# Performance work log

Measured on AMD Instinct MI355X. Metric: run time of the kernel, lower is better.

Reference implementation:

```python
import jax, jax.numpy as jnp
import numpy as np

S, B, D_MODEL, H = 2048, 2, 1024, 16
DH = D_MODEL // H
SCALE = 1.0 / np.sqrt(DH)
NEG_INF = jnp.float32(-1e30)


def setup_inputs() -> dict:
    key = jax.random.key(0)
    ks = jax.random.split(key, 12)
    std = 1.0 / np.sqrt(D_MODEL)
    inp = {
        "query": jax.random.normal(ks[0], (S, B, D_MODEL), jnp.float32),
        "key": jax.random.normal(ks[1], (S, B, D_MODEL), jnp.float32),
        "value": jax.random.normal(ks[2], (S, B, D_MODEL), jnp.float32),
        # causal mask, shape (seq_q, seq_k, 1) per prepare_mask asserts
        "mask": jnp.tril(jnp.ones((S, S), dtype=bool))[:, :, None],
        # params stored (in, out) for x @ W
        "Wq": jax.random.normal(ks[3], (D_MODEL, H * DH), jnp.float32) * std,
        "bq": jnp.zeros((H * DH,), jnp.float32),
        "Wk": jax.random.normal(ks[4], (D_MODEL, H * DH), jnp.float32) * std,
        "bk": jnp.zeros((H * DH,), jnp.float32),
        "Wv": jax.random.normal(ks[5], (D_MODEL, H * DH), jnp.float32) * std,
        "bv": jnp.zeros((H * DH,), jnp.float32),
        "Wo": jax.random.normal(ks[6], (D_MODEL, D_MODEL), jnp.float32) * std,
        "bo": jnp.zeros((D_MODEL,), jnp.float32),
    }
    return inp


def reference(query, key, value, mask, Wq, bq, Wk, bk, Wv, bv, Wo, bo):
    seq_len, batch, _ = query.shape
    # project and split heads: (S, B, H, DH)
    q = (query @ Wq + bq).reshape(seq_len, batch, H, DH)
    k = (key @ Wk + bk).reshape(key.shape[0], batch, H, DH)
    v = (value @ Wv + bv).reshape(value.shape[0], batch, H, DH)
    # scores: (seq_q, batch, heads, seq_k)
    scores = jnp.einsum("ibhd,jbhd->ibhj", q, k) * SCALE
    # mask (seq_q, seq_k, batch_or_1) -> broadcast to (seq_q, batch, 1, seq_k)
    m = jnp.transpose(mask, (0, 2, 1))[:, :, None, :]
    scores = jnp.where(m, scores, NEG_INF)
    attn = jax.nn.softmax(scores, axis=-1)  # dropout_prob=0.0 (eval)
    x = jnp.einsum("ibhj,jbhd->ibhd", attn, v)
    x = x.reshape(seq_len, batch, H * DH)
    return x @ Wo + bo
```

## Files before the change

### kernel.cpp

```cpp
#include <hip/hip_runtime.h>
#include <hip/hip_bf16.h>
#include <cstdint>

#define S_LEN 2048
#define BATCH 2
#define DM    1024
#define NH    16
#define DH    64

typedef short s8v __attribute__((ext_vector_type(8)));
typedef float f4v __attribute__((ext_vector_type(4)));
typedef unsigned int u32x2 __attribute__((ext_vector_type(2)));

__device__ __forceinline__ ushort f2bf(float x) {
  union { float f; uint32_t u; } v; v.f = x;
  uint32_t r = v.u + 0x7fffu + ((v.u >> 16) & 1u);
  return (ushort)(r >> 16);
}
__device__ __forceinline__ float bf2f(ushort u) {
  union { uint32_t u; float f; } v; v.u = (uint32_t)u << 16; return v.f;
}
__device__ __forceinline__ uint32_t fbits(float x) {
  union { float f; uint32_t u; } v; v.f = x; return v.u;
}
__device__ __forceinline__ uint32_t bfrnd(uint32_t u) {
  return u + 0x7fffu + ((u >> 16) & 1u);
}
__device__ __forceinline__ uint32_t packbf(uint32_t flo, uint32_t fhi) {
  return __builtin_amdgcn_perm(bfrnd(fhi), bfrnd(flo), 0x07060302u);
}
__device__ __forceinline__ uint32_t packbf_tr(float lo, float hi) {
  return __builtin_amdgcn_perm(fbits(hi), fbits(lo), 0x07060302u);
}

typedef __attribute__((address_space(1))) const void gas_void;
typedef __attribute__((address_space(3))) void las_void;
__device__ __forceinline__ void gld16(void* l, const void* g) {
  __builtin_amdgcn_global_load_lds((gas_void*)(uintptr_t)g,
                                   (las_void*)(uintptr_t)l, 16, 0, 0);
}

__global__ __launch_bounds__(256)
void prep(const float* W0, const float* W1, const float* W2, const float* W3,
          ushort* T0, ushort* T1, ushort* T2, ushort* T3,
          const float* X0, const float* X1, const float* X2,
          ushort* O0, ushort* O1, ushort* O2) {
  const int z = blockIdx.z;
  if (z < 4) {
    if (blockIdx.x >= 1024) return;
    const float* W = z == 0 ? W0 : z == 1 ? W1 : z == 2 ? W2 : W3;
    ushort*      T = z == 0 ? T0 : z == 1 ? T1 : z == 2 ? T2 : T3;
    __shared__ ushort tile[32][33];
    const int n0 = (blockIdx.x & 31) * 32, k0 = (blockIdx.x >> 5) * 32;
    const int tx = threadIdx.x & 31, ty = threadIdx.x >> 5;
    #pragma unroll
    for (int r = ty; r < 32; r += 8)
      tile[r][tx] = f2bf(W[(size_t)(k0 + r) * DM + n0 + tx]);
    __syncthreads();
    #pragma unroll
    for (int r = ty; r < 32; r += 8)
      T[(size_t)(n0 + r) * DM + k0 + tx] = tile[tx][r];
  } else {
    const float* X = z == 4 ? X0 : z == 5 ? X1 : X2;
    ushort*      O = z == 4 ? O0 : z == 5 ? O1 : O2;
    const size_t i = ((size_t)blockIdx.x * 256 + threadIdx.x) * 4;
    const float4 v = *(const float4*)(X + i);
    ushort4 h;
    h.x = f2bf(v.x); h.y = f2bf(v.y); h.z = f2bf(v.z); h.w = f2bf(v.w);
    *(ushort4*)(O + i) = h;
  }
}

__global__ __launch_bounds__(256, 2)
void gemm_qkv(const ushort* __restrict__ Xq, const ushort* __restrict__ Xk,
              const ushort* __restrict__ Xv,
              const ushort* __restrict__ Wqt, const ushort* __restrict__ Wkt,
              const ushort* __restrict__ Wvt,
              const float* __restrict__ bq, const float* __restrict__ bk,
              const float* __restrict__ bv,
              ushort* __restrict__ Qh, ushort* __restrict__ Kh,
              ushort* __restrict__ Vt) {
  const int z = blockIdx.z;
  const ushort* A    = z == 0 ? Xq  : z == 1 ? Xk  : Xv;
  const ushort* Bt   = z == 0 ? Wqt : z == 1 ? Wkt : Wvt;
  const float*  bias = z == 0 ? bq  : z == 1 ? bk  : bv;

  __shared__ __align__(16) ushort lds[32768];

  const int tid = threadIdx.x, lane = tid & 63, w = tid >> 6;
  const int wm = w >> 1, wn = w & 1;
  const int lrow = lane & 15, quad = lane >> 4;
  const int m0 = blockIdx.x * 128, n0 = blockIdx.y * 128;

  const int sr4 = lane >> 2;
  const int scol = ((lane & 3) ^ ((lane >> 3) & 3)) * 8;
  const ushort* gA[2]; const ushort* gB[2];
  int dA[2], dB[2];
  #pragma unroll
  for (int t = 0; t < 2; t++) {
    const int c = 2 * w + t;
    gA[t] = A  + (size_t)(m0 + c * 16 + sr4) * DM + scol;
    dA[t] = c * 512;
    gB[t] = Bt + (size_t)(n0 + c * 16 + sr4) * DM + scol;
    dB[t] = 4096 + c * 512;
  }

  const int fr = (lrow >> 1) & 3;
  int pa[4], pb[4];
  #pragma unroll
  for (int i = 0; i < 4; i++) {
    pa[i] = (wm * 64 + i * 16 + lrow) * 32 + ((quad ^ fr) * 8);
    pb[i] = 4096 + (wn * 64 + i * 16 + lrow) * 32 + ((quad ^ fr) * 8);
  }

  f4v acc[4][4];
  #pragma unroll
  for (int i = 0; i < 4; i++)
    #pragma unroll
    for (int j = 0; j < 4; j++)
      acc[i][j] = f4v{0.f, 0.f, 0.f, 0.f};

  #pragma unroll
  for (int t = 0; t < 3; t++) {
    const int bb = t * 8192, ko = t * 32;
    gld16(&lds[bb + dA[0]], gA[0] + ko);
    gld16(&lds[bb + dA[1]], gA[1] + ko);
    gld16(&lds[bb + dB[0]], gB[0] + ko);
    gld16(&lds[bb + dB[1]], gB[1] + ko);
  }
  asm volatile("s_waitcnt vmcnt(8)" ::: "memory");
  __builtin_amdgcn_s_barrier();

  for (int t = 0; t < 32; t++) {
    const int bb = (t & 3) * 8192;
    const bool st = t < 29;
    const int sbb = ((t + 3) & 3) * 8192;
    const int ko = (t + 3) * 32;
    s8v af[4], bf[4];
    #pragma unroll
    for (int i = 0; i < 4; i++) af[i] = *(const s8v*)&lds[bb + pa[i]];
    #pragma unroll
    for (int j = 0; j < 4; j++) bf[j] = *(const s8v*)&lds[bb + pb[j]];
    if (st) { gld16(&lds[sbb + dA[0]], gA[0] + ko); gld16(&lds[sbb + dA[1]], gA[1] + ko); }
    __builtin_amdgcn_s_barrier();
    __builtin_amdgcn_s_setprio(1);
    #pragma unroll
    for (int i = 0; i < 2; i++)
      #pragma unroll
      for (int j = 0; j < 4; j++)
        acc[i][j] = __builtin_amdgcn_mfma_f32_16x16x32_bf16(af[i], bf[j], acc[i][j], 0, 0, 0);
    __builtin_amdgcn_s_setprio(0);
    __builtin_amdgcn_s_barrier();
    if (st) { gld16(&lds[sbb + dB[0]], gB[0] + ko); gld16(&lds[sbb + dB[1]], gB[1] + ko); }
    __builtin_amdgcn_s_barrier();
    __builtin_amdgcn_s_setprio(1);
    #pragma unroll
    for (int i = 2; i < 4; i++)
      #pragma unroll
      for (int j = 0; j < 4; j++)
        acc[i][j] = __builtin_amdgcn_mfma_f32_16x16x32_bf16(af[i], bf[j], acc[i][j], 0, 0, 0);
    __builtin_amdgcn_s_setprio(0);
    if (t < 29)       asm volatile("s_waitcnt vmcnt(8)" ::: "memory");
    else if (t == 29) asm volatile("s_waitcnt vmcnt(4)" ::: "memory");
    else if (t == 30) asm volatile("s_waitcnt vmcnt(0)" ::: "memory");
    __builtin_amdgcn_s_barrier();
  }

  if (z <= 1) {
    ushort* O = (z == 0) ? Qh : Kh;
    #pragma unroll
    for (int i = 0; i < 4; i++)
      #pragma unroll
      for (int j = 0; j < 4; j++) {
        const int n = n0 + wn * 64 + j * 16 + lrow;
        const float bval = bias[n];
        const int h = n >> 6, d = n & 63;
        const int mb = m0 + wm * 64 + i * 16 + quad * 4;
        #pragma unroll
        for (int r = 0; r < 4; r++) {
          const int m = mb + r;
          O[((size_t)((m & 1) * NH + h) * S_LEN + (m >> 1)) * DH + d] = f2bf(acc[i][j][r] + bval);
        }
      }
  } else {
    ushort* tw = lds + w * 5120;
    const int h = (n0 + wn * 64) >> 6;
    const int s0 = (m0 + wm * 64) >> 1;
    #pragma unroll
    for (int i = 0; i < 4; i++)
      #pragma unroll
      for (int j = 0; j < 4; j++) {
        const int d_l = j * 16 + lrow;
        const float bval = bias[n0 + wn * 64 + d_l];
        const f4v a = acc[i][j];
        const int sbase = i * 8 + quad * 2;
        const uint32_t p0 = packbf(fbits(a[0] + bval), fbits(a[2] + bval));
        const uint32_t p1 = packbf(fbits(a[1] + bval), fbits(a[3] + bval));
        *(uint32_t*)&tw[d_l * 40 + sbase]        = p0;
        *(uint32_t*)&tw[2560 + d_l * 40 + sbase] = p1;
      }
    #pragma unroll
    for (int b = 0; b < 2; b++)
      #pragma unroll
      for (int p = 0; p < 4; p++) {
        const int d_l = p * 16 + (lane >> 2);
        const int c   = lane & 3;
        const s8v v = *(const s8v*)&tw[b * 2560 + d_l * 40 + c * 8];
        *(s8v*)&Vt[((size_t)(b * NH + h) * DH + d_l) * S_LEN + s0 + c * 8] = v;
      }
  }
}

__global__ __launch_bounds__(256)
void attn(const ushort* __restrict__ Qh, const ushort* __restrict__ Kh,
          const ushort* __restrict__ Vt, ushort* __restrict__ X,
          ushort* __restrict__ Opart, float* __restrict__ lpart) {
  __shared__ __align__(16) ushort lds[3 * 8192];

  const int tid = threadIdx.x, lane = tid & 63, w = tid >> 6;
  const int lrow = lane & 15, quad = lane >> 4;
  const int bh = blockIdx.x;
  const int slot = blockIdx.y;
  int qt, part, nparts;
  if (slot < 18)      { qt = 15 - slot / 3;        part = slot % 3;        nparts = 3; }
  else if (slot < 30) { qt = 9  - (slot - 18) / 2; part = (slot - 18) % 2; nparts = 2; }
  else                { qt = 33 - slot;            part = 0;               nparts = 1; }
  const int nj  = 2 * qt + 2;
  const int jlo = part * nj / nparts;
  const int jhi = (part + 1) * nj / nparts;
  const int iw  = qt * 128 + w * 32;

  const int srow = lane >> 3;
  const int scol = ((lane & 7) ^ srow) * 8;
  const ushort* gK0 = Kh + ((size_t)bh * S_LEN + 2 * w * 8 + srow) * DH + scol;
  const ushort* gK1 = gK0 + 8 * DH;
  const ushort* gV0 = Vt + ((size_t)bh * DH + 2 * w * 8 + srow) * S_LEN + scol;
  const ushort* gV1 = gV0 + 8 * S_LEN;
  const int lK0 = 2 * w * 512, lK1 = lK0 + 512;
  const int lV0 = 4096 + 2 * w * 512, lV1 = lV0 + 512;

  s8v aq[2][2];
  #pragma unroll
  for (int is = 0; is < 2; is++)
    #pragma unroll
    for (int kk = 0; kk < 2; kk++)
      aq[is][kk] = *(const s8v*)(Qh + ((size_t)bh * S_LEN + iw + is * 16 + lrow) * DH +
                                 kk * 32 + quad * 8);

  const int f8 = lrow & 7;
  int pk[4][2], pv[4][2];
  #pragma unroll
  for (int s4 = 0; s4 < 4; s4++)
    #pragma unroll
    for (int kk = 0; kk < 2; kk++) {
      pk[s4][kk] = (s4 * 16 + lrow) * 64 + (((kk * 4 + quad) ^ f8) * 8);
      pv[s4][kk] = 4096 + (s4 * 16 + lrow) * 64 + (((kk * 4 + quad) ^ f8) * 8);
    }

  f4v o[2][4];
  f4v lacc[2];
  #pragma unroll
  for (int is = 0; is < 2; is++) {
    lacc[is] = f4v{0.f, 0.f, 0.f, 0.f};
    #pragma unroll
    for (int d4 = 0; d4 < 4; d4++) o[is][d4] = f4v{0.f, 0.f, 0.f, 0.f};
  }
  const s8v vones = {0x3F80, 0x3F80, 0x3F80, 0x3F80, 0x3F80, 0x3F80, 0x3F80, 0x3F80};

  {
    const int b0 = (jlo % 3) * 8192;
    const size_t j0 = (size_t)jlo * 64;
    gld16(&lds[b0 + lK0], gK0 + j0 * DH);
    gld16(&lds[b0 + lK1], gK1 + j0 * DH);
    gld16(&lds[b0 + lV0], gV0 + j0);
    gld16(&lds[b0 + lV1], gV1 + j0);
    if (jlo + 1 < jhi) {
      const int b1 = ((jlo + 1) % 3) * 8192;
      const size_t j1 = (size_t)(jlo + 1) * 64;
      gld16(&lds[b1 + lK0], gK0 + j1 * DH);
      gld16(&lds[b1 + lK1], gK1 + j1 * DH);
      gld16(&lds[b1 + lV0], gV0 + j1);
      gld16(&lds[b1 + lV1], gV1 + j1);
    }
  }

  int bcur = jlo % 3;
  for (int jt = jlo; jt < jhi; jt++) {
    const int j0 = jt * 64;
    if (jt + 1 < jhi) asm volatile("s_waitcnt vmcnt(4)" ::: "memory");
    else              asm volatile("s_waitcnt vmcnt(0)" ::: "memory");
    __builtin_amdgcn_s_barrier();
    const int cur = bcur * 8192;
    if (jt + 2 < jhi) {
      const int sb = (bcur == 0 ? 2 : bcur - 1) * 8192;
      const size_t jn = (size_t)(jt + 2) * 64;
      gld16(&lds[sb + lK0], gK0 + jn * DH);
      gld16(&lds[sb + lK1], gK1 + jn * DH);
      gld16(&lds[sb + lV0], gV0 + jn);
      gld16(&lds[sb + lV1], gV1 + jn);
    }
    bcur = (bcur == 2) ? 0 : bcur + 1;
    if (j0 > iw + 31) continue;

    f4v sc[2][4];
    #pragma unroll
    for (int is = 0; is < 2; is++)
      #pragma unroll
      for (int s4 = 0; s4 < 4; s4++) sc[is][s4] = f4v{0.f, 0.f, 0.f, 0.f};
    __builtin_amdgcn_s_setprio(1);
    #pragma unroll
    for (int s4 = 0; s4 < 4; s4++) {
      const s8v k0f = *(const s8v*)&lds[cur + pk[s4][0]];
      const s8v k1f = *(const s8v*)&lds[cur + pk[s4][1]];
      sc[0][s4] = __builtin_amdgcn_mfma_f32_16x16x32_bf16(k0f, aq[0][0], sc[0][s4], 0, 0, 0);
      sc[1][s4] = __builtin_amdgcn_mfma_f32_16x16x32_bf16(k0f, aq[1][0], sc[1][s4], 0, 0, 0);
      sc[0][s4] = __builtin_amdgcn_mfma_f32_16x16x32_bf16(k1f, aq[0][1], sc[0][s4], 0, 0, 0);
      sc[1][s4] = __builtin_amdgcn_mfma_f32_16x16x32_bf16(k1f, aq[1][1], sc[1][s4], 0, 0, 0);
    }
    __builtin_amdgcn_s_setprio(0);

    const bool needmask = (j0 + 63) > iw;
    const float C = 0.18033688011112042f;
    uint32_t sw[2][4][2];
    #pragma unroll
    for (int is = 0; is < 2; is++) {
      const int ig = iw + is * 16 + lrow;
      #pragma unroll
      for (int s4 = 0; s4 < 4; s4++) {
        float e0 = __builtin_amdgcn_exp2f(sc[is][s4][0] * C);
        float e1 = __builtin_amdgcn_exp2f(sc[is][s4][1] * C);
        float e2 = __builtin_amdgcn_exp2f(sc[is][s4][2] * C);
        float e3 = __builtin_amdgcn_exp2f(sc[is][s4][3] * C);
        if (needmask) {
          const int jb = j0 + s4 * 16 + quad * 4;
          e0 = (jb + 0 > ig) ? 0.f : e0;
          e1 = (jb + 1 > ig) ? 0.f : e1;
          e2 = (jb + 2 > ig) ? 0.f : e2;
          e3 = (jb + 3 > ig) ? 0.f : e3;
        }
        sw[is][s4][0] = packbf_tr(e0, e1);
        sw[is][s4][1] = packbf_tr(e2, e3);
      }
    }

    s8v ap[2][2];
    #pragma unroll
    for (int is = 0; is < 2; is++)
      #pragma unroll
      for (int kt = 0; kt < 2; kt++) {
        const u32x2 a32 = __builtin_amdgcn_permlane32_swap(
            sw[is][2 * kt][0], sw[is][2 * kt + 1][0], false, false);
        const u32x2 a16 = __builtin_amdgcn_permlane16_swap(a32[0], a32[1], false, false);
        const u32x2 b32 = __builtin_amdgcn_permlane32_swap(
            sw[is][2 * kt][1], sw[is][2 * kt + 1][1], false, false);
        const u32x2 b16 = __builtin_amdgcn_permlane16_swap(b32[0], b32[1], false, false);
        union { uint32_t u[4]; s8v v; } cvt;
        cvt.u[0] = a16[0]; cvt.u[1] = b16[0]; cvt.u[2] = a16[1]; cvt.u[3] = b16[1];
        ap[is][kt] = cvt.v;
      }

    __builtin_amdgcn_s_setprio(1);
    #pragma unroll
    for (int d4 = 0; d4 < 4; d4++) {
      const s8v v0 = *(const s8v*)&lds[cur + pv[d4][0]];
      const s8v v1 = *(const s8v*)&lds[cur + pv[d4][1]];
      o[0][d4] = __builtin_amdgcn_mfma_f32_16x16x32_bf16(ap[0][0], v0, o[0][d4], 0, 0, 0);
      o[1][d4] = __builtin_amdgcn_mfma_f32_16x16x32_bf16(ap[1][0], v0, o[1][d4], 0, 0, 0);
      o[0][d4] = __builtin_amdgcn_mfma_f32_16x16x32_bf16(ap[0][1], v1, o[0][d4], 0, 0, 0);
      o[1][d4] = __builtin_amdgcn_mfma_f32_16x16x32_bf16(ap[1][1], v1, o[1][d4], 0, 0, 0);
    }
    lacc[0] = __builtin_amdgcn_mfma_f32_16x16x32_bf16(ap[0][0], vones, lacc[0], 0, 0, 0);
    lacc[0] = __builtin_amdgcn_mfma_f32_16x16x32_bf16(ap[0][1], vones, lacc[0], 0, 0, 0);
    lacc[1] = __builtin_amdgcn_mfma_f32_16x16x32_bf16(ap[1][0], vones, lacc[1], 0, 0, 0);
    lacc[1] = __builtin_amdgcn_mfma_f32_16x16x32_bf16(ap[1][1], vones, lacc[1], 0, 0, 0);
    __builtin_amdgcn_s_setprio(0);
  }

  if (nparts == 1) {
    const int bb = bh >> 4, h = bh & 15;
    #pragma unroll
    for (int is = 0; is < 2; is++)
      #pragma unroll
      for (int r = 0; r < 4; r++) {
        const float inv = 1.0f / lacc[is][r];
        const int sg = iw + is * 16 + quad * 4 + r;
        #pragma unroll
        for (int d4 = 0; d4 < 4; d4++)
          X[((size_t)sg * BATCH + bb) * DM + h * DH + d4 * 16 + lrow] =
              f2bf(o[is][d4][r] * inv);
      }
  } else {
    ushort* Op = Opart + ((size_t)(bh * 30 + slot) * 128 + w * 32) * 64;
    #pragma unroll
    for (int is = 0; is < 2; is++)
      #pragma unroll
      for (int r = 0; r < 4; r++) {
        const int row_l = is * 16 + quad * 4 + r;
        #pragma unroll
        for (int d4 = 0; d4 < 4; d4++)
          Op[row_l * 64 + d4 * 16 + lrow] = f2bf(o[is][d4][r]);
      }
    if (lrow == 0) {
      float* lp = lpart + (size_t)(bh * 30 + slot) * 128 + w * 32;
      #pragma unroll
      for (int is = 0; is < 2; is++)
        #pragma unroll
        for (int r = 0; r < 4; r++)
          lp[is * 16 + quad * 4 + r] = lacc[is][r];
    }
  }
}

__global__ __launch_bounds__(256)
void combine(const ushort* __restrict__ Opart, const float* __restrict__ lpart,
             ushort* __restrict__ X) {
  const uint32_t gid = blockIdx.x * 256 + threadIdx.x;
  const int dv   = gid & 15;
  const int row  = (gid >> 4) & 127;
  const int rest = gid >> 11;
  const int qi   = rest % 12;
  const int bh   = rest / 12;
  const int qt   = 4 + qi;
  int s0, c;
  if (qt >= 10) { s0 = 3 * (15 - qt); c = 3; }
  else          { s0 = 18 + 2 * (9 - qt); c = 2; }

  float a0 = 0.f, a1 = 0.f, a2 = 0.f, a3 = 0.f, l = 0.f;
  #pragma unroll
  for (int p = 0; p < 3; p++) {
    if (p < c) {
      const size_t base = ((size_t)(bh * 30 + s0 + p) * 128 + row);
      const ushort4 v = *(const ushort4*)&Opart[base * 64 + dv * 4];
      a0 += bf2f(v.x); a1 += bf2f(v.y); a2 += bf2f(v.z); a3 += bf2f(v.w);
      l += lpart[base];
    }
  }
  const float inv = 1.0f / l;
  const int qpos = qt * 128 + row;
  const int b = bh >> 4, h = bh & 15;
  ushort4 hv;
  hv.x = f2bf(a0 * inv);
  hv.y = f2bf(a1 * inv);
  hv.z = f2bf(a2 * inv);
  hv.w = f2bf(a3 * inv);
  *(ushort4*)&X[(((size_t)qpos * BATCH + b) * NH + h) * DH + dv * 4] = hv;
}

__global__ __launch_bounds__(256, 2)
void gemm_out(const ushort* __restrict__ A, const ushort* __restrict__ Bt,
              const float* __restrict__ bias, float* __restrict__ C) {
  __shared__ __align__(16) ushort lds[32768];

  const int tid = threadIdx.x, lane = tid & 63, w = tid >> 6;
  const int wm = w >> 1, wn = w & 1;
  const int lrow = lane & 15, quad = lane >> 4;
  const int m0 = blockIdx.x * 128, n0 = blockIdx.y * 128;

  const int sr4 = lane >> 2;
  const int scol = ((lane & 3) ^ ((lane >> 3) & 3)) * 8;
  const ushort* gA[2]; const ushort* gB[2];
  int dA[2], dB[2];
  #pragma unroll
  for (int t = 0; t < 2; t++) {
    const int c = 2 * w + t;
    gA[t] = A  + (size_t)(m0 + c * 16 + sr4) * DM + scol;
    dA[t] = c * 512;
    gB[t] = Bt + (size_t)(n0 + c * 16 + sr4) * DM + scol;
    dB[t] = 4096 + c * 512;
  }

  const int fr = (lrow >> 1) & 3;
  int pa[4], pb[4];
  #pragma unroll
  for (int i = 0; i < 4; i++) {
    pa[i] = (wm * 64 + i * 16 + lrow) * 32 + ((quad ^ fr) * 8);
    pb[i] = 4096 + (wn * 64 + i * 16 + lrow) * 32 + ((quad ^ fr) * 8);
  }

  f4v acc[4][4];
  #pragma unroll
  for (int i = 0; i < 4; i++)
    #pragma unroll
    for (int j = 0; j < 4; j++)
      acc[i][j] = f4v{0.f, 0.f, 0.f, 0.f};

  #pragma unroll
  for (int t = 0; t < 3; t++) {
    const int bb = t * 8192, ko = t * 32;
    gld16(&lds[bb + dA[0]], gA[0] + ko);
    gld16(&lds[bb + dA[1]], gA[1] + ko);
    gld16(&lds[bb + dB[0]], gB[0] + ko);
    gld16(&lds[bb + dB[1]], gB[1] + ko);
  }
  asm volatile("s_waitcnt vmcnt(8)" ::: "memory");
  __builtin_amdgcn_s_barrier();

  for (int t = 0; t < 32; t++) {
    const int bb = (t & 3) * 8192;
    const bool st = t < 29;
    const int sbb = ((t + 3) & 3) * 8192;
    const int ko = (t + 3) * 32;
    s8v af[4], bf[4];
    #pragma unroll
    for (int i = 0; i < 4; i++) af[i] = *(const s8v*)&lds[bb + pa[i]];
    #pragma unroll
    for (int j = 0; j < 4; j++) bf[j] = *(const s8v*)&lds[bb + pb[j]];
    if (st) { gld16(&lds[sbb + dA[0]], gA[0] + ko); gld16(&lds[sbb + dA[1]], gA[1] + ko); }
    __builtin_amdgcn_s_barrier();
    __builtin_amdgcn_s_setprio(1);
    #pragma unroll
    for (int i = 0; i < 2; i++)
      #pragma unroll
      for (int j = 0; j < 4; j++)
        acc[i][j] = __builtin_amdgcn_mfma_f32_16x16x32_bf16(af[i], bf[j], acc[i][j], 0, 0, 0);
    __builtin_amdgcn_s_setprio(0);
    __builtin_amdgcn_s_barrier();
    if (st) { gld16(&lds[sbb + dB[0]], gB[0] + ko); gld16(&lds[sbb + dB[1]], gB[1] + ko); }
    __builtin_amdgcn_s_barrier();
    __builtin_amdgcn_s_setprio(1);
    #pragma unroll
    for (int i = 2; i < 4; i++)
      #pragma unroll
      for (int j = 0; j < 4; j++)
        acc[i][j] = __builtin_amdgcn_mfma_f32_16x16x32_bf16(af[i], bf[j], acc[i][j], 0, 0, 0);
    __builtin_amdgcn_s_setprio(0);
    if (t < 29)       asm volatile("s_waitcnt vmcnt(8)" ::: "memory");
    else if (t == 29) asm volatile("s_waitcnt vmcnt(4)" ::: "memory");
    else if (t == 30) asm volatile("s_waitcnt vmcnt(0)" ::: "memory");
    __builtin_amdgcn_s_barrier();
  }

  #pragma unroll
  for (int i = 0; i < 4; i++)
    #pragma unroll
    for (int j = 0; j < 4; j++) {
      const int n = n0 + wn * 64 + j * 16 + lrow;
      const float bval = bias[n];
      const int mb = m0 + wm * 64 + i * 16 + quad * 4;
      #pragma unroll
      for (int r = 0; r < 4; r++)
        C[(size_t)(mb + r) * DM + n] = acc[i][j][r] + bval;
    }
}

extern "C" void kernel_launch(void* const* d_in, const int* in_sizes, int n_in,
                              void* d_out, int out_size, void* d_ws, size_t ws_size,
                              hipStream_t stream) {
  const float* query = (const float*)d_in[0];
  const float* key_  = (const float*)d_in[1];
  const float* value = (const float*)d_in[2];
  const float* Wq = (const float*)d_in[4];
  const float* bq = (const float*)d_in[5];
  const float* Wk = (const float*)d_in[6];
  const float* bk = (const float*)d_in[7];
  const float* Wv = (const float*)d_in[8];
  const float* bv = (const float*)d_in[9];
  const float* Wo = (const float*)d_in[10];
  const float* bo = (const float*)d_in[11];

  ushort* Wqt = (ushort*)d_ws;
  ushort* Wkt = Wqt + (size_t)1024 * 1024;
  ushort* Wvt = Wkt + (size_t)1024 * 1024;
  ushort* Wot = Wvt + (size_t)1024 * 1024;
  ushort* Xbq = Wot + (size_t)1024 * 1024;
  ushort* Xbk = Xbq + (size_t)4 * 1024 * 1024;
  ushort* Xbv = Xbk + (size_t)4 * 1024 * 1024;
  ushort* Qh  = Xbv + (size_t)4 * 1024 * 1024;
  ushort* Kh  = Qh  + (size_t)4 * 1024 * 1024;
  ushort* Vt  = Kh  + (size_t)4 * 1024 * 1024;
  ushort* Opart = Xbk;
  float*  lpart = (float*)Wqt;
  ushort* Xa  = Xbq;

  prep<<<dim3(4096, 1, 7), 256, 0, stream>>>(Wq, Wk, Wv, Wo, Wqt, Wkt, Wvt, Wot,
                                             query, key_, value, Xbq, Xbk, Xbv);
  gemm_qkv<<<dim3(32, 8, 3), 256, 0, stream>>>(Xbq, Xbk, Xbv,
                                               Wqt, Wkt, Wvt, bq, bk, bv,
                                               Qh, Kh, Vt);
  attn<<<dim3(32, 34), 256, 0, stream>>>(Qh, Kh, Vt, Xa, Opart, lpart);
  combine<<<3072, 256, 0, stream>>>(Opart, lpart, Xa);
  gemm_out<<<dim3(32, 8), 256, 0, stream>>>(Xa, Wot, bo, (float*)d_out);
}
```

Before: 223.1 us.

## Fold softmax scale into Q projection and switch attention to double-buffered LDS

The constant scale times log2(e) is now applied to Q when the projection kernel writes it, which removes one multiply per score before exp2 in the attention loop. The attention kernel's K/V staging drops from three LDS buffers to two, prefetching one tile ahead with a full vmcnt(0) wait each iteration. This lowers LDS use per block, which may allow more resident blocks. The cost is less load latency hidden per iteration, and rounding the pre-scaled Q to bf16 slightly changes numerics.

```diff
diff --git a/kernel.cpp b/kernel.cpp
--- a/kernel.cpp
+++ b/kernel.cpp
@@ -168,6 +168,7 @@
 
   if (z <= 1) {
     ushort* O = (z == 0) ? Qh : Kh;
+    const float qs = (z == 0) ? 0.18033688011112042f : 1.0f;
     #pragma unroll
     for (int i = 0; i < 4; i++)
       #pragma unroll
@@ -179,7 +180,8 @@
         #pragma unroll
         for (int r = 0; r < 4; r++) {
           const int m = mb + r;
-          O[((size_t)((m & 1) * NH + h) * S_LEN + (m >> 1)) * DH + d] = f2bf(acc[i][j][r] + bval);
+          O[((size_t)((m & 1) * NH + h) * S_LEN + (m >> 1)) * DH + d] =
+              f2bf((acc[i][j][r] + bval) * qs);
         }
       }
   } else {
@@ -215,7 +217,7 @@
 void attn(const ushort* __restrict__ Qh, const ushort* __restrict__ Kh,
           const ushort* __restrict__ Vt, ushort* __restrict__ X,
           ushort* __restrict__ Opart, float* __restrict__ lpart) {
-  __shared__ __align__(16) ushort lds[3 * 8192];
+  __shared__ __align__(16) ushort lds[2 * 8192];
 
   const int tid = threadIdx.x, lane = tid & 63, w = tid >> 6;
   const int lrow = lane & 15, quad = lane >> 4;
@@ -268,38 +270,27 @@
   const s8v vones = {0x3F80, 0x3F80, 0x3F80, 0x3F80, 0x3F80, 0x3F80, 0x3F80, 0x3F80};
 
   {
-    const int b0 = (jlo % 3) * 8192;
+    const int b0 = (jlo & 1) * 8192;
     const size_t j0 = (size_t)jlo * 64;
     gld16(&lds[b0 + lK0], gK0 + j0 * DH);
     gld16(&lds[b0 + lK1], gK1 + j0 * DH);
     gld16(&lds[b0 + lV0], gV0 + j0);
     gld16(&lds[b0 + lV1], gV1 + j0);
-    if (jlo + 1 < jhi) {
-      const int b1 = ((jlo + 1) % 3) * 8192;
-      const size_t j1 = (size_t)(jlo + 1) * 64;
-      gld16(&lds[b1 + lK0], gK0 + j1 * DH);
-      gld16(&lds[b1 + lK1], gK1 + j1 * DH);
-      gld16(&lds[b1 + lV0], gV0 + j1);
-      gld16(&lds[b1 + lV1], gV1 + j1);
-    }
-  }
-
-  int bcur = jlo % 3;
+  }
+
   for (int jt = jlo; jt < jhi; jt++) {
     const int j0 = jt * 64;
-    if (jt + 1 < jhi) asm volatile("s_waitcnt vmcnt(4)" ::: "memory");
-    else              asm volatile("s_waitcnt vmcnt(0)" ::: "memory");
-    __builtin_amdgcn_s_barrier();
-    const int cur = bcur * 8192;
-    if (jt + 2 < jhi) {
-      const int sb = (bcur == 0 ? 2 : bcur - 1) * 8192;
-      const size_t jn = (size_t)(jt + 2) * 64;
-      gld16(&lds[sb + lK0], gK0 + jn * DH);
-      gld16(&lds[sb + lK1], gK1 + jn * DH);
-      gld16(&lds[sb + lV0], gV0 + jn);
-      gld16(&lds[sb + lV1], gV1 + jn);
-    }
-    bcur = (bcur == 2) ? 0 : bcur + 1;
+    asm volatile("s_waitcnt vmcnt(0)" ::: "memory");
+    __builtin_amdgcn_s_barrier();
+    const int cur = (jt & 1) * 8192;
+    if (jt + 1 < jhi) {
+      const int nb = ((jt + 1) & 1) * 8192;
+      const size_t jn = (size_t)(jt + 1) * 64;
+      gld16(&lds[nb + lK0], gK0 + jn * DH);
+      gld16(&lds[nb + lK1], gK1 + jn * DH);
+      gld16(&lds[nb + lV0], gV0 + jn);
+      gld16(&lds[nb + lV1], gV1 + jn);
+    }
     if (j0 > iw + 31) continue;
 
     f4v sc[2][4];
@@ -320,17 +311,16 @@
     __builtin_amdgcn_s_setprio(0);
 
     const bool needmask = (j0 + 63) > iw;
-    const float C = 0.18033688011112042f;
     uint32_t sw[2][4][2];
     #pragma unroll
     for (int is = 0; is < 2; is++) {
       const int ig = iw + is * 16 + lrow;
       #pragma unroll
       for (int s4 = 0; s4 < 4; s4++) {
-        float e0 = __builtin_amdgcn_exp2f(sc[is][s4][0] * C);
-        float e1 = __builtin_amdgcn_exp2f(sc[is][s4][1] * C);
-        float e2 = __builtin_amdgcn_exp2f(sc[is][s4][2] * C);
-        float e3 = __builtin_amdgcn_exp2f(sc[is][s4][3] * C);
+        float e0 = __builtin_amdgcn_exp2f(sc[is][s4][0]);
+        float e1 = __builtin_amdgcn_exp2f(sc[is][s4][1]);
+        float e2 = __builtin_amdgcn_exp2f(sc[is][s4][2]);
+        float e3 = __builtin_amdgcn_exp2f(sc[is][s4][3]);
         if (needmask) {
           const int jb = j0 + s4 * 16 + quad * 4;
           e0 = (jb + 0 > ig) ? 0.f : e0;
```

New measurement: 218.2 us. -2.2%, faster.
